# Optimization experiments

Measured on AMD Instinct MI355X. Metric: run time of the kernel, lower is better.

## Reference

```python
import jax, jax.numpy as jnp
import numpy as np

HEADS = 4
HEAD_DIM = 24
FOLD = 2   # fold_w = fold_h = fold_d
PROP = 2   # proposal_w = proposal_h = proposal_d


def _conv1x1(x, w, b):
    # x: [B,Cin,W,H,D], w: [Cout,Cin] -> [B,Cout,W,H,D]  (1x1x1 Conv3d)
    return jnp.einsum('bcwhd,oc->bowhd', x, w) + b[None, :, None, None, None]


def _fold(t, f):
    # 'b c (f1 w)(f2 h)(f3 d) -> (b f1 f2 f3) c w h d'
    b, c, W, H, D = t.shape
    w, h, d = W // f, H // f, D // f
    t = t.reshape(b, c, f, w, f, h, f, d)
    t = t.transpose(0, 2, 4, 6, 1, 3, 5, 7)
    return t.reshape(b * f * f * f, c, w, h, d)


def _unfold(t, f):
    # '(b f1 f2 f3) c w h d -> b c (f1 w)(f2 h)(f3 d)'
    bf, c, w, h, d = t.shape
    b = bf // (f * f * f)
    t = t.reshape(b, f, f, f, c, w, h, d)
    t = t.transpose(0, 4, 1, 5, 2, 6, 3, 7)
    return t.reshape(b, c, f * w, f * h, f * d)


def _adaptive_pool(t, p):
    # AdaptiveAvgPool3d((p,p,p)) with divisible spatial dims == block mean
    b, c, W, H, D = t.shape
    t = t.reshape(b, c, p, W // p, p, H // p, p, D // p)
    return t.mean(axis=(3, 5, 7))


def _normalize(v, eps=1e-12):
    n = jnp.linalg.norm(v, axis=-1, keepdims=True)
    return v / jnp.maximum(n, eps)


def setup_inputs() -> dict:
    key = jax.random.key(0)
    ks = jax.random.split(key, 4)
    B, C, W = 4, 96, 32
    inner = HEADS * HEAD_DIM  # 96
    return {
        'x': jax.random.normal(ks[0], (B, C, W, W, W), jnp.float32),
        'f_w': jax.random.normal(ks[1], (inner, C), jnp.float32) * 0.02,
        'f_b': jnp.zeros((inner,), jnp.float32),
        'v_w': jax.random.normal(ks[2], (inner, C), jnp.float32) * 0.02,
        'v_b': jnp.zeros((inner,), jnp.float32),
        'proj_w': jax.random.normal(ks[3], (C, inner), jnp.float32) * 0.02,
        'proj_b': jnp.zeros((C,), jnp.float32),
        'sim_alpha': jnp.ones((1,), jnp.float32),
        'sim_beta': jnp.zeros((1,), jnp.float32),
    }


def reference(x, f_w, f_b, v_w, v_b, proj_w, proj_b, sim_alpha, sim_beta):
    value = _conv1x1(x, v_w, v_b)
    feat = _conv1x1(x, f_w, f_b)

    def split_heads(t):  # 'b (e c) whd -> (b e) c whd'
        b, C = t.shape[:2]
        return t.reshape(b * HEADS, C // HEADS, *t.shape[2:])

    feat = split_heads(feat)
    value = split_heads(value)
    feat = _fold(feat, FOLD)
    value = _fold(value, FOLD)

    b, c, w, h, d = feat.shape
    N = w * h * d
    M = PROP ** 3
    centers = _adaptive_pool(feat, PROP)  # [b,c,p,p,p]
    value_centers = _adaptive_pool(value, PROP).reshape(b, c, M).transpose(0, 2, 1)  # [b,M,c]

    cflat = centers.reshape(b, c, M).transpose(0, 2, 1)  # [b,M,c]
    xflat = feat.reshape(b, c, N).transpose(0, 2, 1)     # [b,N,c]
    sim = jax.nn.sigmoid(sim_beta + sim_alpha *
                         jnp.einsum('bmc,bnc->bmn', _normalize(cflat), _normalize(xflat)))  # [b,M,N]
    idx = jnp.argmax(sim, axis=1)  # [b,N] hard assignment (first max, like torch)
    mask = (jnp.arange(M)[None, :, None] == idx[:, None, :]).astype(sim.dtype)
    sim = sim * mask

    value2 = value.reshape(b, c, N).transpose(0, 2, 1)  # [b,N,c]
    agg = (jnp.einsum('bmn,bnc->bmc', sim, value2) + value_centers) / (sim.sum(-1, keepdims=True) + 1.0)
    out = jnp.einsum('bmc,bmn->bnc', agg, sim)  # dispatch back to points
    out = out.transpose(0, 2, 1).reshape(b, c, w, h, d)

    out = _unfold(out, FOLD)
    bb = out.shape[0] // HEADS  # '(b e) c -> b (e c)'
    out = out.reshape(bb, HEADS * c, *out.shape[2:])
    out = _conv1x1(out, proj_w, proj_b)
    return out
```

## Files before the change

kernel.cpp:

```cpp
#include <hip/hip_runtime.h>
#include <hip/hip_bf16.h>


__global__ __launch_bounds__(256) void k0_prep(
    const float* __restrict__ fw, const float* __restrict__ vw,
    const float* __restrict__ pw, float* __restrict__ wfT,
    float* __restrict__ wvT, float* __restrict__ wpT)
{
    int t = blockIdx.x * 256 + threadIdx.x;
    if (t < 96 * 96) {
        int o = t / 96, c = t % 96;
        wfT[c * 96 + o] = fw[o * 96 + c];
        wvT[c * 96 + o] = vw[o * 96 + c];
        wpT[c * 96 + o] = pw[o * 96 + c];
    }
}

__global__ __launch_bounds__(256) void k_pool(
    const float* __restrict__ x, double* __restrict__ xmeanD)
{
    int gid = blockIdx.x * 256 + threadIdx.x;
    int bc = gid >> 6;
    int b = bc / 96, c = bc - b * 96;
    int fm = gid & 63;
    int f1 = (fm >> 5) & 1, f2 = (fm >> 4) & 1, f3 = (fm >> 3) & 1, m = fm & 7;
    int W0 = f1 * 16 + (m >> 2) * 8;
    int H0 = f2 * 16 + ((m >> 1) & 1) * 8;
    int D0 = f3 * 16 + (m & 1) * 8;
    const float* xb = x + ((size_t)b * 96 + c) * 32768;
    double s = 0.0;
    for (int iw = 0; iw < 8; ++iw)
        for (int ih = 0; ih < 8; ++ih) {
            const float4* p = (const float4*)(xb + (W0 + iw) * 1024 + (H0 + ih) * 32 + D0);
            float4 a = p[0], q = p[1];
            s += (double)a.x + (double)a.y + (double)a.z + (double)a.w
               + (double)q.x + (double)q.y + (double)q.z + (double)q.w;
        }
    xmeanD[(size_t)(b * 64 + fm) * 96 + c] = s * (1.0 / 512.0);
}

__global__ __launch_bounds__(192) void k_cent(
    const float* __restrict__ fw, const float* __restrict__ fb,
    const float* __restrict__ vw, const float* __restrict__ vb,
    const double* __restrict__ xmeanD, double* __restrict__ chat,
    float* __restrict__ vcent)
{
    __shared__ double centL[8][24];
    __shared__ double dnv[8];
    const int B2 = blockIdx.x, t = threadIdx.x;
    const int mm = t / 24, co = t - mm * 24;
    const int b = B2 >> 5, g = (B2 >> 3) & 3, fff = B2 & 7;
    const int ob = g * 24;
    const double* xm = xmeanD + (size_t)(b * 64 + fff * 8 + mm) * 96;
    double cF = (double)fb[ob + co];
    float  cV = vb[ob + co];
    const float* fr = fw + (ob + co) * 96;
    const float* vr = vw + (ob + co) * 96;
    for (int ci = 0; ci < 96; ++ci) {
        double xv = xm[ci];
        cF += (double)fr[ci] * xv;
        cV += vr[ci] * (float)xv;
    }
    centL[mm][co] = cF;
    __syncthreads();
    if (t < 8) {
        double ss = 0.0;
        #pragma unroll
        for (int cc = 0; cc < 24; ++cc) ss += centL[t][cc] * centL[t][cc];
        dnv[t] = fmax(sqrt(ss), 1e-12);
    }
    __syncthreads();
    chat[(size_t)B2 * 192 + mm * 24 + co] = cF / dnv[mm];
    vcent[(size_t)B2 * 192 + t] = cV;
}

__global__ __launch_bounds__(256) void k_prep_u(
    const float* __restrict__ fw, const float* __restrict__ fb,
    const double* __restrict__ chat, double* __restrict__ uG)
{
    int gid = blockIdx.x * 256 + threadIdx.x;
    if (gid >= 128 * 776) return;
    int B2 = gid / 776, rem = gid - B2 * 776;
    int c = rem >> 3, m = rem & 7;
    int g = (B2 >> 3) & 3;
    const double* ch = chat + (size_t)B2 * 192 + m * 24;
    double s = 0.0;
    if (c < 96) {
        for (int o = 0; o < 24; ++o) s += (double)fw[(g * 24 + o) * 96 + c] * ch[o];
    } else {
        for (int o = 0; o < 24; ++o) s += (double)fb[g * 24 + o] * ch[o];
    }
    uG[(size_t)B2 * 776 + c * 8 + m] = s;
}

__global__ __launch_bounds__(256) void k1_conv(
    const float* __restrict__ x, const float* __restrict__ wfT,
    const float* __restrict__ fb, const double* __restrict__ uG,
    const float* __restrict__ al, const float* __restrict__ be,
    float* __restrict__ svb, unsigned char* __restrict__ bmb)
{
    __shared__ float xt[96][64];
    const int tile = blockIdx.x;
    const int b = tile >> 9;
    const int r = tile & 511;
    const int W = r >> 4;
    const int Hq = (r >> 1) & 7;
    const int f3 = r & 1;
    const int f1 = W >> 4, f2 = Hq >> 2;
    const float* xb = x + (size_t)b * 96 * 32768 + W * 1024 + Hq * 4 * 32 + f3 * 16;

    #pragma unroll
    for (int k = 0; k < 24; ++k) {
        int idx = k * 256 + threadIdx.x;
        int c = idx >> 6, i2 = idx & 63;
        xt[c][i2] = xb[(size_t)c * 32768 + (i2 >> 4) * 32 + (i2 & 15)];
    }
    __syncthreads();

    const int i = threadIdx.x & 63;
    const int g = threadIdx.x >> 6;
    const int ob = __builtin_amdgcn_readfirstlane(g * 24);
    const int B2 = (b << 5) | (g << 3) | (f1 << 2) | (f2 << 1) | f3;
    const int uoff = __builtin_amdgcn_readfirstlane(B2 * 776);
    const double* ug = uG + uoff;

    double a[8];
    #pragma unroll
    for (int m = 0; m < 8; ++m) a[m] = ug[768 + m];
    float accN[24];
    #pragma unroll
    for (int oo = 0; oo < 24; ++oo) accN[oo] = fb[ob + oo];

    for (int c = 0; c < 96; ++c) {
        const float xv = xt[c][i];
        const double xd = (double)xv;
        const double* uc = ug + c * 8;
        #pragma unroll
        for (int m = 0; m < 8; ++m) a[m] = fma(xd, uc[m], a[m]);
        const float* wr = wfT + c * 96 + ob;
        #pragma unroll
        for (int oo = 0; oo < 24; ++oo) accN[oo] = fmaf(xv, wr[oo], accN[oo]);
    }

    float ss = 0.f;
    #pragma unroll
    for (int oo = 0; oo < 24; ++oo) ss = fmaf(accN[oo], accN[oo], ss);
    const float dn = fmaxf(sqrtf(ss), 1e-12f);

    const double alpha = (double)al[0];
    const double beta  = (double)be[0];
    int bm = 0; double dbest = a[0];
    if (alpha > 0.0) {
        #pragma unroll
        for (int m = 1; m < 8; ++m) if (a[m] > dbest) { dbest = a[m]; bm = m; }
    } else if (alpha < 0.0) {
        #pragma unroll
        for (int m = 1; m < 8; ++m) if (a[m] < dbest) { dbest = a[m]; bm = m; }
    }
    const double tv = beta + alpha * (dbest / (double)dn);
    const float sv = 1.f / (1.f + expf(-(float)tv));

    const int n = ((W & 15) << 8) | (((Hq & 3) * 4 + (i >> 4)) << 4) | (i & 15);
    svb[(size_t)B2 * 4096 + n] = sv;
    bmb[(size_t)B2 * 4096 + n] = (unsigned char)bm;
}

__global__ __launch_bounds__(256) void k_xagg(
    const float* __restrict__ x, const float* __restrict__ svb,
    const unsigned char* __restrict__ bmb, float* __restrict__ xagg,
    float* __restrict__ cntb)
{
    __shared__ float red[256][33];
    __shared__ float red2[8][32];
    const int grp = blockIdx.x / 97;
    const int c   = blockIdx.x - grp * 97;
    const int b = grp >> 3, fff = grp & 7;
    const int f1 = fff >> 2, f2 = (fff >> 1) & 1, f3 = fff & 1;
    const int t = threadIdx.x;
    const float* xc = x + ((size_t)b * 96 + (c < 96 ? c : 0)) * 32768;
    const int sbase = f1 * 16 * 1024 + f2 * 16 * 32 + f3 * 16;

    float acc[4][8];
    #pragma unroll
    for (int g = 0; g < 4; ++g)
        #pragma unroll
        for (int m = 0; m < 8; ++m) acc[g][m] = 0.f;

    #pragma unroll 4
    for (int k = 0; k < 16; ++k) {
        const int n = k * 256 + t;
        const int s = sbase + (n >> 8) * 1024 + ((n >> 4) & 15) * 32 + (n & 15);
        const float xv = (c < 96) ? xc[s] : 1.0f;
        #pragma unroll
        for (int g = 0; g < 4; ++g) {
            const int B2g = (b << 5) | (g << 3) | fff;
            const float svv = svb[(size_t)B2g * 4096 + n];
            const int bmv = bmb[(size_t)B2g * 4096 + n];
            const float p = svv * xv;
            #pragma unroll
            for (int m = 0; m < 8; ++m)
                acc[g][m] += (bmv == m) ? p : 0.f;
        }
    }

    #pragma unroll
    for (int g = 0; g < 4; ++g)
        #pragma unroll
        for (int m = 0; m < 8; ++m) red[t][g * 8 + m] = acc[g][m];
    __syncthreads();
    {
        const int j = t & 31, part = t >> 5;
        float s = 0.f;
        #pragma unroll
        for (int kk = 0; kk < 32; ++kk) s += red[part * 32 + kk][j];
        red2[part][j] = s;
    }
    __syncthreads();
    if (t < 32) {
        float s = 0.f;
        #pragma unroll
        for (int p = 0; p < 8; ++p) s += red2[p][t];
        const int g = t >> 3, m = t & 7;
        const int B2g = (b << 5) | (g << 3) | fff;
        if (c < 96) xagg[((size_t)B2g * 8 + m) * 96 + c] = s;
        else        cntb[B2g * 8 + m] = s;
    }
}

__global__ __launch_bounds__(256) void k_pagg(
    const float* __restrict__ wvT, const float* __restrict__ vb,
    const float* __restrict__ wpT, const float* __restrict__ xagg,
    const float* __restrict__ cntb, const float* __restrict__ vcent,
    float* __restrict__ pagg)
{
    __shared__ float xa_l[8][96];
    __shared__ float agg_l[8][25];
    __shared__ float cnt_l[8];
    const int B2 = blockIdx.x, t = threadIdx.x;
    const int g = (B2 >> 3) & 3;
    for (int k = t; k < 768; k += 256) ((float*)xa_l)[k] = xagg[(size_t)B2 * 768 + k];
    if (t < 8) cnt_l[t] = cntb[B2 * 8 + t];
    __syncthreads();
    if (t < 192) {
        const int m = t / 24, o = t - m * 24;
        float s = 0.f;
        for (int ci = 0; ci < 96; ++ci)
            s = fmaf(wvT[ci * 96 + g * 24 + o], xa_l[m][ci], s);
        s += cnt_l[m] * vb[g * 24 + o] + vcent[(size_t)B2 * 192 + t];
        agg_l[m][o] = s / (cnt_l[m] + 1.f);
    }
    __syncthreads();
    #pragma unroll
    for (int r = 0; r < 3; ++r) {
        const int k = r * 256 + t;
        const int m = k / 96, C = k - m * 96;
        float s = 0.f;
        #pragma unroll
        for (int o = 0; o < 24; ++o)
            s = fmaf(wpT[(g * 24 + o) * 96 + C], agg_l[m][o], s);
        pagg[(size_t)B2 * 768 + k] = s;
    }
}

__global__ __launch_bounds__(256) void k_disp(
    const float* __restrict__ pagg, const float* __restrict__ svb,
    const unsigned char* __restrict__ bmb, const float* __restrict__ pb,
    float* __restrict__ out)
{
    __shared__ float pagg_l[4][776];
    __shared__ float svs[4][64];
    __shared__ unsigned char bms[4][64];
    const int tile = blockIdx.x;
    const int b = tile >> 9;
    const int r = tile & 511;
    const int W = r >> 4;
    const int Hq = (r >> 1) & 7;
    const int f3 = r & 1;
    const int f1 = W >> 4, f2 = Hq >> 2;
    const int t = threadIdx.x;
    const int i = t & 63, q = t >> 6;

    const int n = ((W & 15) << 8) | ((((Hq & 3) << 2) | (i >> 4)) << 4) | (i & 15);
    {
        const int B2q = (b << 5) | (q << 3) | (f1 << 2) | (f2 << 1) | f3;
        svs[q][i] = svb[(size_t)B2q * 4096 + n];
        bms[q][i] = bmb[(size_t)B2q * 4096 + n];
    }
    for (int k = t; k < 3072; k += 256) {
        const int g = k >> 10;
        const int gg = k / 768, rem = k - gg * 768;
        const int m = rem / 96, c = rem - m * 96;
        const int B2g = (b << 5) | (gg << 3) | (f1 << 2) | (f2 << 1) | f3;
        (void)g;
        pagg_l[gg][m * 97 + c] = pagg[(size_t)B2g * 768 + rem];
    }
    __syncthreads();

    const int co = q * 24;
    float acc[24];
    #pragma unroll
    for (int oo = 0; oo < 24; ++oo) acc[oo] = pb[co + oo];
    #pragma unroll
    for (int g = 0; g < 4; ++g) {
        const float sv = svs[g][i];
        const int bm = bms[g][i];
        const float* pg = &pagg_l[g][bm * 97 + co];
        #pragma unroll
        for (int oo = 0; oo < 24; ++oo) acc[oo] = fmaf(sv, pg[oo], acc[oo]);
    }
    const int s = W * 1024 + ((Hq << 2) | (i >> 4)) * 32 + f3 * 16 + (i & 15);
    #pragma unroll
    for (int oo = 0; oo < 24; ++oo)
        out[((size_t)b * 96 + co + oo) * 32768 + s] = acc[oo];
}

extern "C" void kernel_launch(void* const* d_in, const int* in_sizes, int n_in,
                              void* d_out, int out_size, void* d_ws, size_t ws_size,
                              hipStream_t stream)
{
    const float* x  = (const float*)d_in[0];
    const float* fw = (const float*)d_in[1];
    const float* fb = (const float*)d_in[2];
    const float* vw = (const float*)d_in[3];
    const float* vb = (const float*)d_in[4];
    const float* pw = (const float*)d_in[5];
    const float* pb = (const float*)d_in[6];
    const float* al = (const float*)d_in[7];
    const float* be = (const float*)d_in[8];
    float* out = (float*)d_out;

    char* ws = (char*)d_ws;
    float*  wfT   = (float*)(ws);
    float*  wpT   = (float*)(ws + 36864);
    float*  wvT   = (float*)(ws + 73728);
    double* xmeanD= (double*)(ws + 110592);
    double* chat  = (double*)(ws + 307200);
    double* uG    = (double*)(ws + 503808);
    float*  vcent = (float*)(ws + 1298432);
    float*  xagg  = (float*)(ws + 1396736);
    float*  cntb  = (float*)(ws + 1789952);
    float*  pagg  = (float*)(ws + 1794048);
    float*  svb   = (float*)(ws + 2187264);
    unsigned char* bmb = (unsigned char*)(ws + 4284416);

    k0_prep<<<36, 256, 0, stream>>>(fw, vw, pw, wfT, wvT, wpT);
    k_pool<<<96, 256, 0, stream>>>(x, xmeanD);
    k_cent<<<128, 192, 0, stream>>>(fw, fb, vw, vb, xmeanD, chat, vcent);
    k_prep_u<<<388, 256, 0, stream>>>(fw, fb, chat, uG);
    k1_conv<<<2048, 256, 0, stream>>>(x, wfT, fb, uG, al, be, svb, bmb);
    k_xagg<<<3104, 256, 0, stream>>>(x, svb, bmb, xagg, cntb);
    k_pagg<<<128, 256, 0, stream>>>(wvT, vb, wpT, xagg, cntb, vcent, pagg);
    k_disp<<<2048, 256, 0, stream>>>(pagg, svb, bmb, pb, out);
}
```

Before: 248.8 us.

## Merge prep kernels, restructure pooling reduction, and halve conv shared tile

Fuses the weight-transpose and pooling kernels into one launch, and the center and u-precompute kernels into another, dropping two launches and the chat buffer round trip. Pooling now uses one block per (batch, channel) that reads contiguous float4 rows and reduces with wavefront shuffles, instead of 96 small blocks with strided 8x8x8 reads. The conv kernel loads x in two 48-channel halves with float4 loads into a smaller shared tile, which lowers LDS use and may allow higher occupancy. The price is an extra barrier per half in the conv kernel and fewer parallel threads in the fused u computation.

```diff
diff --git a/kernel.cpp b/kernel.cpp
--- a/kernel.cpp
+++ b/kernel.cpp
@@ -2,66 +2,83 @@
 #include <hip/hip_bf16.h>
 
 
-__global__ __launch_bounds__(256) void k0_prep(
+__global__ __launch_bounds__(256) void kA_prep_pool(
     const float* __restrict__ fw, const float* __restrict__ vw,
-    const float* __restrict__ pw, float* __restrict__ wfT,
-    float* __restrict__ wvT, float* __restrict__ wpT)
-{
-    int t = blockIdx.x * 256 + threadIdx.x;
-    if (t < 96 * 96) {
-        int o = t / 96, c = t % 96;
-        wfT[c * 96 + o] = fw[o * 96 + c];
-        wvT[c * 96 + o] = vw[o * 96 + c];
-        wpT[c * 96 + o] = pw[o * 96 + c];
-    }
-}
-
-__global__ __launch_bounds__(256) void k_pool(
-    const float* __restrict__ x, double* __restrict__ xmeanD)
-{
-    int gid = blockIdx.x * 256 + threadIdx.x;
-    int bc = gid >> 6;
-    int b = bc / 96, c = bc - b * 96;
-    int fm = gid & 63;
-    int f1 = (fm >> 5) & 1, f2 = (fm >> 4) & 1, f3 = (fm >> 3) & 1, m = fm & 7;
-    int W0 = f1 * 16 + (m >> 2) * 8;
-    int H0 = f2 * 16 + ((m >> 1) & 1) * 8;
-    int D0 = f3 * 16 + (m & 1) * 8;
+    const float* __restrict__ pw, const float* __restrict__ x,
+    float* __restrict__ wfT, float* __restrict__ wvT, float* __restrict__ wpT,
+    double* __restrict__ xmeanD)
+{
+    const int bid = blockIdx.x;
+    const int t = threadIdx.x;
+    if (bid < 36) {
+        int k = bid * 256 + t;
+        if (k < 96 * 96) {
+            int o = k / 96, c = k % 96;
+            wfT[c * 96 + o] = fw[o * 96 + c];
+            wvT[c * 96 + o] = vw[o * 96 + c];
+            wpT[c * 96 + o] = pw[o * 96 + c];
+        }
+        return;
+    }
+    const int bc = bid - 36;
+    const int b = bc / 96, c = bc - b * 96;
     const float* xb = x + ((size_t)b * 96 + c) * 32768;
-    double s = 0.0;
-    for (int iw = 0; iw < 8; ++iw)
-        for (int ih = 0; ih < 8; ++ih) {
-            const float4* p = (const float4*)(xb + (W0 + iw) * 1024 + (H0 + ih) * 32 + D0);
-            float4 a = p[0], q = p[1];
-            s += (double)a.x + (double)a.y + (double)a.z + (double)a.w
-               + (double)q.x + (double)q.y + (double)q.z + (double)q.w;
-        }
-    xmeanD[(size_t)(b * 64 + fm) * 96 + c] = s * (1.0 / 512.0);
-}
-
-__global__ __launch_bounds__(192) void k_cent(
+
+    double acc[4];
+    #pragma unroll
+    for (int a = 0; a < 4; ++a) acc[a] = 0.0;
+    #pragma unroll 8
+    for (int k = 0; k < 32; ++k) {
+        float4 v = *(const float4*)(xb + k * 1024 + t * 4);
+        double sc = (double)v.x + (double)v.y + (double)v.z + (double)v.w;
+        acc[k >> 3] += sc;
+    }
+    #pragma unroll
+    for (int a = 0; a < 4; ++a) {
+        acc[a] += __shfl_xor(acc[a], 1);
+        acc[a] += __shfl_xor(acc[a], 8);
+        acc[a] += __shfl_xor(acc[a], 16);
+        acc[a] += __shfl_xor(acc[a], 32);
+    }
+    if ((t & 0x39) == 0) {
+        const int m_D = (t >> 1) & 1, f3 = (t >> 2) & 1;
+        const int m_H = (t >> 6) & 1, f2 = (t >> 7) & 1;
+        #pragma unroll
+        for (int a = 0; a < 4; ++a) {
+            const int f1 = a >> 1, m_W = a & 1;
+            const int fm = f1 * 32 + f2 * 16 + f3 * 8 + m_W * 4 + m_H * 2 + m_D;
+            xmeanD[(size_t)(b * 64 + fm) * 96 + c] = acc[a] * (1.0 / 512.0);
+        }
+    }
+}
+
+__global__ __launch_bounds__(256) void kB_cent_u(
     const float* __restrict__ fw, const float* __restrict__ fb,
     const float* __restrict__ vw, const float* __restrict__ vb,
-    const double* __restrict__ xmeanD, double* __restrict__ chat,
+    const double* __restrict__ xmeanD, double* __restrict__ uG,
     float* __restrict__ vcent)
 {
     __shared__ double centL[8][24];
+    __shared__ double chL[8][24];
     __shared__ double dnv[8];
     const int B2 = blockIdx.x, t = threadIdx.x;
-    const int mm = t / 24, co = t - mm * 24;
     const int b = B2 >> 5, g = (B2 >> 3) & 3, fff = B2 & 7;
     const int ob = g * 24;
-    const double* xm = xmeanD + (size_t)(b * 64 + fff * 8 + mm) * 96;
-    double cF = (double)fb[ob + co];
-    float  cV = vb[ob + co];
-    const float* fr = fw + (ob + co) * 96;
-    const float* vr = vw + (ob + co) * 96;
-    for (int ci = 0; ci < 96; ++ci) {
-        double xv = xm[ci];
-        cF += (double)fr[ci] * xv;
-        cV += vr[ci] * (float)xv;
-    }
-    centL[mm][co] = cF;
+    if (t < 192) {
+        const int mm = t / 24, co = t - mm * 24;
+        const double* xm = xmeanD + (size_t)(b * 64 + fff * 8 + mm) * 96;
+        double cF = (double)fb[ob + co];
+        float  cV = vb[ob + co];
+        const float* fr = fw + (ob + co) * 96;
+        const float* vr = vw + (ob + co) * 96;
+        for (int ci = 0; ci < 96; ++ci) {
+            double xv = xm[ci];
+            cF += (double)fr[ci] * xv;
+            cV += vr[ci] * (float)xv;
+        }
+        centL[mm][co] = cF;
+        vcent[(size_t)B2 * 192 + t] = cV;
+    }
     __syncthreads();
     if (t < 8) {
         double ss = 0.0;
@@ -70,27 +87,23 @@
         dnv[t] = fmax(sqrt(ss), 1e-12);
     }
     __syncthreads();
-    chat[(size_t)B2 * 192 + mm * 24 + co] = cF / dnv[mm];
-    vcent[(size_t)B2 * 192 + t] = cV;
-}
-
-__global__ __launch_bounds__(256) void k_prep_u(
-    const float* __restrict__ fw, const float* __restrict__ fb,
-    const double* __restrict__ chat, double* __restrict__ uG)
-{
-    int gid = blockIdx.x * 256 + threadIdx.x;
-    if (gid >= 128 * 776) return;
-    int B2 = gid / 776, rem = gid - B2 * 776;
-    int c = rem >> 3, m = rem & 7;
-    int g = (B2 >> 3) & 3;
-    const double* ch = chat + (size_t)B2 * 192 + m * 24;
-    double s = 0.0;
-    if (c < 96) {
-        for (int o = 0; o < 24; ++o) s += (double)fw[(g * 24 + o) * 96 + c] * ch[o];
-    } else {
-        for (int o = 0; o < 24; ++o) s += (double)fb[g * 24 + o] * ch[o];
-    }
-    uG[(size_t)B2 * 776 + c * 8 + m] = s;
+    if (t < 192) {
+        const int mm = t / 24, co = t - mm * 24;
+        chL[mm][co] = centL[mm][co] / dnv[mm];
+    }
+    __syncthreads();
+    for (int k = t; k < 776; k += 256) {
+        const int c = k >> 3, m = k & 7;
+        double s = 0.0;
+        if (c < 96) {
+            #pragma unroll
+            for (int o = 0; o < 24; ++o) s += (double)fw[(ob + o) * 96 + c] * chL[m][o];
+        } else {
+            #pragma unroll
+            for (int o = 0; o < 24; ++o) s += (double)fb[ob + o] * chL[m][o];
+        }
+        uG[(size_t)B2 * 776 + k] = s;
+    }
 }
 
 __global__ __launch_bounds__(256) void k1_conv(
@@ -99,7 +112,7 @@
     const float* __restrict__ al, const float* __restrict__ be,
     float* __restrict__ svb, unsigned char* __restrict__ bmb)
 {
-    __shared__ float xt[96][64];
+    __shared__ float xt[48][64];
     const int tile = blockIdx.x;
     const int b = tile >> 9;
     const int r = tile & 511;
@@ -107,18 +120,10 @@
     const int Hq = (r >> 1) & 7;
     const int f3 = r & 1;
     const int f1 = W >> 4, f2 = Hq >> 2;
-    const float* xb = x + (size_t)b * 96 * 32768 + W * 1024 + Hq * 4 * 32 + f3 * 16;
-
-    #pragma unroll
-    for (int k = 0; k < 24; ++k) {
-        int idx = k * 256 + threadIdx.x;
-        int c = idx >> 6, i2 = idx & 63;
-        xt[c][i2] = xb[(size_t)c * 32768 + (i2 >> 4) * 32 + (i2 & 15)];
-    }
-    __syncthreads();
-
-    const int i = threadIdx.x & 63;
-    const int g = threadIdx.x >> 6;
+    const float* xbase = x + (size_t)b * 96 * 32768 + W * 1024 + Hq * 128 + f3 * 16;
+    const int t = threadIdx.x;
+    const int i = t & 63;
+    const int g = t >> 6;
     const int ob = __builtin_amdgcn_readfirstlane(g * 24);
     const int B2 = (b << 5) | (g << 3) | (f1 << 2) | (f2 << 1) | f3;
     const int uoff = __builtin_amdgcn_readfirstlane(B2 * 776);
@@ -131,15 +136,29 @@
     #pragma unroll
     for (int oo = 0; oo < 24; ++oo) accN[oo] = fb[ob + oo];
 
-    for (int c = 0; c < 96; ++c) {
-        const float xv = xt[c][i];
-        const double xd = (double)xv;
-        const double* uc = ug + c * 8;
-        #pragma unroll
-        for (int m = 0; m < 8; ++m) a[m] = fma(xd, uc[m], a[m]);
-        const float* wr = wfT + c * 96 + ob;
-        #pragma unroll
-        for (int oo = 0; oo < 24; ++oo) accN[oo] = fmaf(xv, wr[oo], accN[oo]);
+    #pragma unroll
+    for (int half = 0; half < 2; ++half) {
+        const int h0 = half * 48;
+        if (half) __syncthreads();
+        #pragma unroll
+        for (int j = 0; j < 3; ++j) {
+            const int q = j * 256 + t;
+            const int row = q >> 2, e = q & 3;
+            const int cl = row >> 2, hh = row & 3;
+            float4 v = *(const float4*)(xbase + (size_t)(h0 + cl) * 32768 + hh * 32 + e * 4);
+            *(float4*)&xt[cl][hh * 16 + e * 4] = v;
+        }
+        __syncthreads();
+        for (int cl = 0; cl < 48; ++cl) {
+            const float xv = xt[cl][i];
+            const double xd = (double)xv;
+            const double* uc = ug + (h0 + cl) * 8;
+            #pragma unroll
+            for (int m = 0; m < 8; ++m) a[m] = fma(xd, uc[m], a[m]);
+            const float* wr = wfT + (h0 + cl) * 96 + ob;
+            #pragma unroll
+            for (int oo = 0; oo < 24; ++oo) accN[oo] = fmaf(xv, wr[oo], accN[oo]);
+        }
     }
 
     float ss = 0.f;
@@ -287,11 +306,9 @@
         bms[q][i] = bmb[(size_t)B2q * 4096 + n];
     }
     for (int k = t; k < 3072; k += 256) {
-        const int g = k >> 10;
         const int gg = k / 768, rem = k - gg * 768;
         const int m = rem / 96, c = rem - m * 96;
         const int B2g = (b << 5) | (gg << 3) | (f1 << 2) | (f2 << 1) | f3;
-        (void)g;
         pagg_l[gg][m * 97 + c] = pagg[(size_t)B2g * 768 + rem];
     }
     __syncthreads();
@@ -331,22 +348,19 @@
 
     char* ws = (char*)d_ws;
     float*  wfT   = (float*)(ws);
-    float*  wpT   = (float*)(ws + 36864);
-    float*  wvT   = (float*)(ws + 73728);
+    float*  wvT   = (float*)(ws + 36864);
+    float*  wpT   = (float*)(ws + 73728);
     double* xmeanD= (double*)(ws + 110592);
-    double* chat  = (double*)(ws + 307200);
-    double* uG    = (double*)(ws + 503808);
-    float*  vcent = (float*)(ws + 1298432);
-    float*  xagg  = (float*)(ws + 1396736);
-    float*  cntb  = (float*)(ws + 1789952);
-    float*  pagg  = (float*)(ws + 1794048);
-    float*  svb   = (float*)(ws + 2187264);
-    unsigned char* bmb = (unsigned char*)(ws + 4284416);
-
-    k0_prep<<<36, 256, 0, stream>>>(fw, vw, pw, wfT, wvT, wpT);
-    k_pool<<<96, 256, 0, stream>>>(x, xmeanD);
-    k_cent<<<128, 192, 0, stream>>>(fw, fb, vw, vb, xmeanD, chat, vcent);
-    k_prep_u<<<388, 256, 0, stream>>>(fw, fb, chat, uG);
+    double* uG    = (double*)(ws + 307200);
+    float*  vcent = (float*)(ws + 1101824);
+    float*  xagg  = (float*)(ws + 1200128);
+    float*  cntb  = (float*)(ws + 1593344);
+    float*  pagg  = (float*)(ws + 1597440);
+    float*  svb   = (float*)(ws + 1990656);
+    unsigned char* bmb = (unsigned char*)(ws + 4087808);
+
+    kA_prep_pool<<<420, 256, 0, stream>>>(fw, vw, pw, x, wfT, wvT, wpT, xmeanD);
+    kB_cent_u<<<128, 256, 0, stream>>>(fw, fb, vw, vb, xmeanD, uG, vcent);
     k1_conv<<<2048, 256, 0, stream>>>(x, wfT, fb, uG, al, be, svb, bmb);
     k_xagg<<<3104, 256, 0, stream>>>(x, svb, bmb, xagg, cntb);
     k_pagg<<<128, 256, 0, stream>>>(wvT, vb, wpT, xagg, cntb, vcent, pagg);
```

Measured after the change: 239.5 us. 1.04x faster.
